# Kernel tuning notes

Measured on AMD Instinct MI355X. Metric: run time of the kernel, lower is better.

Reference implementation:

```python
import jax, jax.numpy as jnp
import numpy as np

B, S, D = 2, 4096, 1024
H, DK, DV = 4, 128, 256          # head_k_dim, head_v_dim
KD, VD = H * DK, H * DV          # key_dim=512, value_dim=1024
RANK = 16                        # gate_low_rank_dim
GLN = 16.0                       # gate_logit_normalizer
EPS = 1e-5
C = 64                           # chunk size
NC = S // C


def setup_inputs() -> dict:
    key = jax.random.key(0)
    ks = jax.random.split(key, 9)
    w = lambda k, shape: (jax.random.normal(k, shape, jnp.float32) * 0.02)
    return {
        "x": jax.random.normal(ks[0], (B, S, D), jnp.float32),
        "Wq": w(ks[1], (D, KD)),
        "Wk": w(ks[2], (D, KD)),
        "Wv": w(ks[3], (D, VD)),
        "Wgk1": w(ks[4], (D, RANK)),
        "Wgk2": w(ks[5], (RANK, KD)),
        "bgk": jnp.zeros((KD,), jnp.float32),
        "Wg": w(ks[6], (D, VD)),
        "Wo": w(ks[7], (VD, D)),
        "norm_w": jnp.ones((DV,), jnp.float32),
    }


def _gla_chunk(q, k, v, gk):
    """Chunkwise gated linear attention. q,k,gk: [B,S,H,DK]; v: [B,S,H,DV]."""
    qc = q.reshape(B, NC, C, H, DK)
    kc = k.reshape(B, NC, C, H, DK)
    vc = v.reshape(B, NC, C, H, DV)
    gc = gk.reshape(B, NC, C, H, DK)
    gcum = jnp.cumsum(gc, axis=2)                       # inclusive within-chunk cumsum (<= 0)
    g_last = gcum[:, :, -1]                             # [B,NC,H,DK]
    q_t = qc * jnp.exp(gcum)                            # q decayed forward
    k_inv = kc * jnp.exp(-gcum)                         # for intra-chunk scores
    k_dec = kc * jnp.exp(g_last[:, :, None] - gcum)     # for state update (bounded)
    # intra-chunk causal scores
    A = jnp.einsum('bnthk,bnshk->bnhts', q_t, k_inv)    # [B,NC,H,C,C]
    mask = jnp.tril(jnp.ones((C, C), bool))
    A = jnp.where(mask, A, 0.0)
    o_intra = jnp.einsum('bnhts,bnshv->bnthv', A, vc)   # [B,NC,C,H,DV]
    # per-chunk state contribution
    kv = jnp.einsum('bnthk,bnthv->bnhkv', k_dec, vc)    # [B,NC,H,DK,DV]

    def step(state, inp):
        q_tc, gl, kvc = inp                             # [B,C,H,DK], [B,H,DK], [B,H,DK,DV]
        o_inter = jnp.einsum('bthk,bhkv->bthv', q_tc, state)
        state = state * jnp.exp(gl)[..., None] + kvc
        return state, o_inter

    xs = (jnp.swapaxes(q_t, 0, 1), jnp.swapaxes(g_last, 0, 1), jnp.swapaxes(kv, 0, 1))
    init = jnp.zeros((B, H, DK, DV), q.dtype)
    _, o_inter = jax.lax.scan(step, init, xs)           # [NC,B,C,H,DV]
    o = o_intra + jnp.swapaxes(o_inter, 0, 1)
    return o.reshape(B, S, H, DV)


def reference(x, Wq, Wk, Wv, Wgk1, Wgk2, bgk, Wg, Wo, norm_w):
    scale = DK ** -0.5
    q = (x @ Wq).reshape(B, S, H, DK) * scale
    k = (x @ Wk).reshape(B, S, H, DK)
    v = (x @ Wv).reshape(B, S, H, DV)
    gk = (jax.nn.log_sigmoid((x @ Wgk1) @ Wgk2 + bgk) / GLN).reshape(B, S, H, DK)
    o = _gla_chunk(q, k, v, gk)                          # [B,S,H,DV]
    # fused RMSNorm + swish gate (per-head norm over DV)
    g = (x @ Wg).reshape(B, S, H, DV)
    o = o * jax.lax.rsqrt(jnp.mean(o * o, axis=-1, keepdims=True) + EPS) * norm_w
    o = o * (g * jax.nn.sigmoid(g))
    return o.reshape(B, S, VD) @ Wo
```

## Files before the change

kernel.cpp:

```cpp
#include <hip/hip_runtime.h>

typedef __bf16 bf16_t;
typedef __bf16 bf16x8 __attribute__((ext_vector_type(8)));
typedef float  f32x4  __attribute__((ext_vector_type(4)));

#define MFMA16(a,b,c) __builtin_amdgcn_mfma_f32_16x16x32_bf16((a),(b),(c),0,0,0)

#define SCALE_Q 0.08838834764831845f

#define GLOBAL_LOAD_LDS16(gptr, lptr)                                          \
  __builtin_amdgcn_global_load_lds(                                            \
      (const __attribute__((address_space(1))) void*)(gptr),                   \
      (__attribute__((address_space(3))) void*)(lptr), 16, 0, 0)

#define SBAR   __builtin_amdgcn_s_barrier()
#define SCHEDB __builtin_amdgcn_sched_barrier(0)

__global__ __launch_bounds__(256) void k_convert(const void* __restrict__ src,
                                                 const unsigned int* __restrict__ nwp,
                                                 bf16_t* __restrict__ dst, int n) {
  bool isf32 = (nwp[0] == 0x3F800000u);
  int g = blockIdx.x * 256 + threadIdx.x;
  int i = g * 8;
  if (i >= n) return;
  if (isf32) {
    const float4* s = (const float4*)src;
    float4 a = s[g * 2], b = s[g * 2 + 1];
    bf16x8 o;
    o[0] = (bf16_t)a.x; o[1] = (bf16_t)a.y; o[2] = (bf16_t)a.z; o[3] = (bf16_t)a.w;
    o[4] = (bf16_t)b.x; o[5] = (bf16_t)b.y; o[6] = (bf16_t)b.z; o[7] = (bf16_t)b.w;
    *(bf16x8*)(dst + i) = o;
  } else {
    *(bf16x8*)(dst + i) = ((const bf16x8*)src)[g];
  }
}

struct ConvSrcs {
  const void *wq, *wk, *wv, *wg, *wo, *gk1, *gk2, *bgk, *nw;
};
__device__ __forceinline__ void convT_tile(const void* src, bf16_t* dst,
                                           int Ccols, int bx, int by,
                                           bool isf32, bf16_t (*t)[33]) {
  int tx = threadIdx.x & 31, ty = threadIdx.x >> 5;
  int r0 = by * 32, c0 = bx * 32;
#pragma unroll
  for (int i = 0; i < 4; i++) {
    int r = r0 + ty + i * 8, cc = c0 + tx;
    float v = isf32 ? ((const float*)src)[(size_t)r * Ccols + cc]
                    : (float)((const bf16_t*)src)[(size_t)r * Ccols + cc];
    t[ty + i * 8][tx] = (bf16_t)v;
  }
  __syncthreads();
#pragma unroll
  for (int i = 0; i < 4; i++) {
    int cc = c0 + ty + i * 8;
    dst[(size_t)cc * 1024 + r0 + tx] = t[tx][ty + i * 8];
  }
}
__device__ __forceinline__ void conv_straight(const void* src, bf16_t* dst,
                                              int base_blk, int n, bool isf32) {
  int g = (blockIdx.x - base_blk) * 256 + threadIdx.x;
  int i = g * 8;
  if (i >= n) return;
  if (isf32) {
    const float4* s = (const float4*)src;
    float4 a = s[g * 2], b = s[g * 2 + 1];
    bf16x8 o;
    o[0] = (bf16_t)a.x; o[1] = (bf16_t)a.y; o[2] = (bf16_t)a.z; o[3] = (bf16_t)a.w;
    o[4] = (bf16_t)b.x; o[5] = (bf16_t)b.y; o[6] = (bf16_t)b.z; o[7] = (bf16_t)b.w;
    *(bf16x8*)(dst + i) = o;
  } else {
    *(bf16x8*)(dst + i) = ((const bf16x8*)src)[g];
  }
}
__global__ __launch_bounds__(256) void k_convW(ConvSrcs s,
                                               const unsigned int* __restrict__ nwp,
                                               bf16_t* __restrict__ tWcat,
                                               bf16_t* __restrict__ tWo,
                                               bf16_t* __restrict__ cWgk1,
                                               bf16_t* __restrict__ cWgk2,
                                               bf16_t* __restrict__ cbgk,
                                               bf16_t* __restrict__ cnw) {
  __shared__ bf16_t t[32][33];
  bool isf32 = (nwp[0] == 0x3F800000u);
  int blk = blockIdx.x;
  if (blk < 512) {
    convT_tile(s.wq, tWcat, 512, blk & 15, blk >> 4, isf32, t);
  } else if (blk < 1024) {
    int b2 = blk - 512;
    convT_tile(s.wk, tWcat + (size_t)512 * 1024, 512, b2 & 15, b2 >> 4, isf32, t);
  } else if (blk < 2048) {
    int b2 = blk - 1024;
    convT_tile(s.wv, tWcat + (size_t)1024 * 1024, 1024, b2 & 31, b2 >> 5, isf32, t);
  } else if (blk < 3072) {
    int b2 = blk - 2048;
    convT_tile(s.wg, tWcat + (size_t)2048 * 1024, 1024, b2 & 31, b2 >> 5, isf32, t);
  } else if (blk < 4096) {
    int b2 = blk - 3072;
    convT_tile(s.wo, tWo, 1024, b2 & 31, b2 >> 5, isf32, t);
  } else if (blk < 4104) {
    conv_straight(s.gk1, cWgk1, 4096, 16384, isf32);
  } else if (blk < 4108) {
    conv_straight(s.gk2, cWgk2, 4104, 8192, isf32);
  } else if (blk == 4108) {
    conv_straight(s.bgk, cbgk, 4108, 512, isf32);
  } else {
    conv_straight(s.nw, cnw, 4109, 256, isf32);
  }
}

__global__ __launch_bounds__(256) void k_gk1(const bf16_t* __restrict__ x,
                                             const bf16_t* __restrict__ W1,
                                             float* __restrict__ tmp) {
  int wave = threadIdx.x >> 6, lane = threadIdx.x & 63;
  int m = blockIdx.x * 4 + wave;
  const bf16_t* xr = x + (size_t)m * 1024;
  float p[16];
#pragma unroll
  for (int n = 0; n < 16; n++) p[n] = 0.f;
  for (int kk = 0; kk < 16; kk++) {
    int k = kk * 64 + lane;
    float xv = (float)xr[k];
    bf16x8 w0 = *(const bf16x8*)(W1 + k * 16);
    bf16x8 w1 = *(const bf16x8*)(W1 + k * 16 + 8);
#pragma unroll
    for (int j = 0; j < 8; j++) {
      p[j]     += xv * (float)w0[j];
      p[8 + j] += xv * (float)w1[j];
    }
  }
#pragma unroll
  for (int off = 1; off < 64; off <<= 1) {
#pragma unroll
    for (int n = 0; n < 16; n++) p[n] += __shfl_xor(p[n], off, 64);
  }
#pragma unroll
  for (int n = 0; n < 16; n++)
    if (lane == n) tmp[(size_t)m * 16 + n] = p[n];
}

__global__ __launch_bounds__(256) void k_gk2(const float* __restrict__ tmp,
                                             const bf16_t* __restrict__ W2,
                                             const bf16_t* __restrict__ bgk,
                                             float* __restrict__ gcum) {
  int g = blockIdx.x * 256 + threadIdx.x;
  int m = g >> 6;
  int n0 = (g & 63) * 8;
  float acc[8];
#pragma unroll
  for (int j = 0; j < 8; j++) acc[j] = 0.f;
  for (int k = 0; k < 16; k++) {
    float tv = tmp[(size_t)m * 16 + k];
    bf16x8 w = *(const bf16x8*)(W2 + k * 512 + n0);
#pragma unroll
    for (int j = 0; j < 8; j++) acc[j] += tv * (float)w[j];
  }
  int b = m >> 12, s = m & 4095;
  int h = n0 >> 7, dk0 = n0 & 127;
  float* dst = gcum + (((size_t)(b * 4 + h) * 4096 + s) * 128 + dk0);
#pragma unroll
  for (int j = 0; j < 8; j++) {
    float z = acc[j] + (float)bgk[n0 + j];
    float lg = -__logf(1.f + __expf(-z)) * (1.f / 16.f);
    dst[j] = fmaxf(lg, -4.0f);
  }
}

__global__ __launch_bounds__(128) void k_cumsum(float* __restrict__ gcum,
                                                float* __restrict__ glast) {
  int blk = blockIdx.x;
  int dk = threadIdx.x;
  float* base = gcum + (size_t)blk * 8192;
  float run = 0.f;
  for (int t = 0; t < 64; t++) {
    run += base[t * 128 + dk];
    base[t * 128 + dk] = run;
  }
  glast[(size_t)blk * 128 + dk] = run;
}

template <int BM, int BN, int NBN, int MODE>
__global__ __launch_bounds__(512, 2) void k_gemm2(
    const bf16_t* __restrict__ Ag, const bf16_t* __restrict__ Bt,
    const float* __restrict__ gcum, const float* __restrict__ glast,
    bf16_t* __restrict__ qt, bf16_t* __restrict__ kinv,
    bf16_t* __restrict__ kdec, bf16_t* __restrict__ vr,
    bf16_t* __restrict__ gmat, float* __restrict__ fout) {
  constexpr int MT = BM / 2 / 16;
  constexpr int ALDS = BM * 64;
  constexpr int BLDS = BN * 64;
  constexpr int NT = 16;
  extern __shared__ __attribute__((aligned(16))) bf16_t sm[];
  bf16_t* As = sm;
  bf16_t* Bs = sm + 2 * ALDS;

  int tid = threadIdx.x;
  int w = tid >> 6, lane = tid & 63;
  int WM = w >> 2, WN = w & 3;
  int quad = lane >> 4, c = lane & 15;

  int nblk = gridDim.x;
  int bid = blockIdx.x;
  int swz = (bid & 7) * (nblk >> 3) + (bid >> 3);
  int bm = swz / NBN, bn = swz % NBN;
  int m0 = bm * BM, n0 = bn * BN;

  int srow = w * 8 + (lane >> 3);
  int scol = ((lane & 7) ^ (lane >> 3)) * 8;
  const bf16_t* aBase = Ag + (size_t)(m0 + srow) * 1024 + scol;
  const bf16_t* bBase = Bt + (size_t)(n0 + srow) * 1024 + scol;

  auto stage = [&](int t, int buf) {
    int kof = t * 64;
#pragma unroll
    for (int j = 0; j < BM / 64; j++)
      GLOBAL_LOAD_LDS16(aBase + (size_t)j * 64 * 1024 + kof,
                        As + buf * ALDS + j * 4096 + w * 512);
#pragma unroll
    for (int j = 0; j < BN / 64; j++)
      GLOBAL_LOAD_LDS16(bBase + (size_t)j * 64 * 1024 + kof,
                        Bs + buf * BLDS + j * 4096 + w * 512);
  };

  int sx = c & 7;
  int aRowOff[MT], bRowOff[4];
#pragma unroll
  for (int mt = 0; mt < MT; mt++) aRowOff[mt] = (WM * (BM / 2) + mt * 16 + c) * 64;
#pragma unroll
  for (int nt = 0; nt < 4; nt++) bRowOff[nt] = (WN * 64 + nt * 16 + c) * 64;

  f32x4 acc[MT][4] = {};

  stage(0, 0);
  stage(1, 1);

  auto compute = [&](int buf) {
#pragma unroll
    for (int ks = 0; ks < 2; ks++) {
      int so = (((ks << 2) | quad) ^ sx) << 3;
      bf16x8 bfr[4];
#pragma unroll
      for (int nt = 0; nt < 4; nt++)
        bfr[nt] = *(const bf16x8*)(Bs + buf * BLDS + bRowOff[nt] + so);
#pragma unroll
      for (int mt = 0; mt < MT; mt++) {
        bf16x8 af = *(const bf16x8*)(As + buf * ALDS + aRowOff[mt] + so);
#pragma unroll
        for (int nt = 0; nt < 4; nt++)
          acc[mt][nt] = MFMA16(af, bfr[nt], acc[mt][nt]);
      }
    }
  };

#pragma unroll 2
  for (int t = 0; t < NT; t++) {
    if (t < NT - 1) {
      if constexpr (BM == 256)
        asm volatile("s_waitcnt vmcnt(8)" ::: "memory");
      else
        asm volatile("s_waitcnt vmcnt(6)" ::: "memory");
    } else {
      asm volatile("s_waitcnt vmcnt(0)" ::: "memory");
    }
    SCHEDB;
    SBAR;
    SCHEDB;
    __builtin_amdgcn_s_setprio(1);
    compute(t & 1);
    __builtin_amdgcn_s_setprio(0);
    SCHEDB;
    SBAR;
    SCHEDB;
    if (t + 2 < NT) stage(t + 2, t & 1);
  }

  int mwb = m0 + WM * (BM / 2);
  int nwb = n0 + WN * 64;
#pragma unroll
  for (int mt = 0; mt < MT; mt++)
#pragma unroll
    for (int nt = 0; nt < 4; nt++)
#pragma unroll
      for (int r = 0; r < 4; r++) {
        int m = mwb + mt * 16 + quad * 4 + r;
        int n = nwb + nt * 16 + c;
        float v = acc[mt][nt][r];
        if constexpr (MODE == 1) {
          fout[(size_t)m * 1024 + n] = v;
        } else {
          if (n0 < 512) {
            int b = m >> 12, ss = m & 4095, h = n >> 7, dk = n & 127;
            size_t idx = ((size_t)(b * 4 + h) * 4096 + ss) * 128 + dk;
            qt[idx] = (bf16_t)(v * SCALE_Q * __expf(gcum[idx]));
          } else if (n0 < 1024) {
            int nk = n - 512;
            int b = m >> 12, ss = m & 4095, h = nk >> 7, dk = nk & 127;
            size_t idx = ((size_t)(b * 4 + h) * 4096 + ss) * 128 + dk;
            float gc = gcum[idx];
            float gl = glast[((size_t)(b * 4 + h) * 64 + (ss >> 6)) * 128 + dk];
            kinv[idx] = (bf16_t)(v * __expf(fminf(-gc, 30.f)));
            kdec[idx] = (bf16_t)(v * __expf(gl - gc));
          } else if (n0 < 2048) {
            int nv = n - 1024;
            int b = m >> 12, ss = m & 4095, h = nv >> 8, dv = nv & 255;
            vr[((size_t)(b * 4 + h) * 4096 + ss) * 256 + dv] = (bf16_t)v;
          } else {
            gmat[(size_t)m * 1024 + (n - 2048)] = (bf16_t)v;
          }
        }
      }
}

__global__ __launch_bounds__(256) void k_attA(const bf16_t* __restrict__ qt,
                                              const bf16_t* __restrict__ kinv,
                                              bf16_t* __restrict__ Aout) {
  int blk = blockIdx.x;
  size_t cb = (size_t)blk * 8192;
  int tid = threadIdx.x, wave = tid >> 6, lane = tid & 63;
  int quad = lane >> 4, c = lane & 15;
  f32x4 acc[4] = {};
  for (int kk = 0; kk < 128; kk += 32) {
    bf16x8 a = *(const bf16x8*)(qt + cb + (size_t)(wave * 16 + c) * 128 + kk + quad * 8);
#pragma unroll
    for (int nt = 0; nt < 4; nt++) {
      bf16x8 bb = *(const bf16x8*)(kinv + cb + (size_t)(nt * 16 + c) * 128 + kk + quad * 8);
      acc[nt] = MFMA16(a, bb, acc[nt]);
    }
  }
#pragma unroll
  for (int nt = 0; nt < 4; nt++)
#pragma unroll
    for (int r = 0; r < 4; r++) {
      int row = wave * 16 + quad * 4 + r, col = nt * 16 + c;
      Aout[(size_t)blk * 4096 + row * 64 + col] =
          (bf16_t)(col <= row ? acc[nt][r] : 0.f);
    }
}

__global__ __launch_bounds__(256, 3) void k_kv(const bf16_t* __restrict__ kdec,
                                            const bf16_t* __restrict__ vr,
                                            bf16_t* __restrict__ kv) {
  int blk = blockIdx.x;
  __shared__ __attribute__((aligned(16))) bf16_t ls_kd[64 * 128];
  __shared__ __attribute__((aligned(16))) bf16_t ls_v[64 * 256];
  int tid = threadIdx.x, wave = tid >> 6, lane = tid & 63;
  int quad = lane >> 4, c = lane & 15;
  size_t cb = (size_t)blk * 8192;
  size_t cv = (size_t)blk * 16384;
  size_t sb = (size_t)blk * 32768;
#pragma unroll
  for (int j = 0; j < 4; j++) {
    int idx = tid + j * 256;
    int row = idx >> 4, col = (idx & 15) * 8;
    *(bf16x8*)&ls_kd[row * 128 + col] = *(const bf16x8*)(kdec + cb + (size_t)row * 128 + col);
  }
#pragma unroll
  for (int j = 0; j < 8; j++) {
    int idx = tid + j * 256;
    int row = idx >> 5, col = (idx & 31) * 8;
    *(bf16x8*)&ls_v[row * 256 + col] = *(const bf16x8*)(vr + cv + (size_t)row * 256 + col);
  }
  __syncthreads();
  int kbase = (wave >> 1) * 64;
  for (int pos = 0; pos < 2; pos++) {
    int dvbase = (wave & 1) * 64 + pos * 128;
    f32x4 acc[4][4] = {};
    for (int kk = 0; kk < 64; kk += 32) {
      bf16x8 a[4], bb[4];
#pragma unroll
      for (int mt = 0; mt < 4; mt++)
#pragma unroll
        for (int j = 0; j < 8; j++)
          a[mt][j] = ls_kd[(kk + quad * 8 + j) * 128 + kbase + mt * 16 + c];
#pragma unroll
      for (int nt = 0; nt < 4; nt++)
#pragma unroll
        for (int j = 0; j < 8; j++)
          bb[nt][j] = ls_v[(kk + quad * 8 + j) * 256 + dvbase + nt * 16 + c];
#pragma unroll
      for (int mt = 0; mt < 4; mt++)
#pragma unroll
        for (int nt = 0; nt < 4; nt++)
          acc[mt][nt] = MFMA16(a[mt], bb[nt], acc[mt][nt]);
    }
#pragma unroll
    for (int mt = 0; mt < 4; mt++)
#pragma unroll
      for (int nt = 0; nt < 4; nt++)
#pragma unroll
        for (int r = 0; r < 4; r++) {
          int kg = kbase + mt * 16 + quad * 4 + r;
          int dg = dvbase + nt * 16 + c;
          kv[sb + (size_t)kg * 256 + dg] = (bf16_t)acc[mt][nt][r];
        }
  }
}

__global__ __launch_bounds__(256) void k_scan2(bf16_t* __restrict__ states,
                                               const float* __restrict__ glast) {
  int g = blockIdx.x * 256 + threadIdx.x;
  int bh = g >> 15;
  int idx = g & 32767;
  int kg = idx >> 8;
  bf16_t* p = states + (size_t)bh * 64 * 32768 + idx;
  const float* gl = glast + (size_t)bh * 64 * 128 + kg;
  float carry = 0.f;
#pragma unroll 4
  for (int n = 0; n < 64; n++) {
    float kvv = (float)p[(size_t)n * 32768];
    float e = __expf(gl[n * 128]);
    p[(size_t)n * 32768] = (bf16_t)carry;
    carry = carry * e + kvv;
  }
}

__global__ __launch_bounds__(256, 4) void k_o(const bf16_t* __restrict__ qt,
                                           const bf16_t* __restrict__ Amat,
                                           const bf16_t* __restrict__ vr,
                                           const bf16_t* __restrict__ states,
                                           const bf16_t* __restrict__ gmat,
                                           const bf16_t* __restrict__ normw,
                                           bf16_t* __restrict__ ob) {
  int blk = blockIdx.x;
  int bh = blk >> 6, n = blk & 63, b = bh >> 2, h = bh & 3;
  __shared__ __attribute__((aligned(16))) bf16_t ls[64 * 256];
  __shared__ __attribute__((aligned(16))) float lred[64][4];
  int tid = threadIdx.x, wave = tid >> 6, lane = tid & 63;
  int quad = lane >> 4, c = lane & 15;
  size_t cb = (size_t)blk * 8192;
  size_t cv = (size_t)blk * 16384;
  size_t sb = (size_t)blk * 32768;
  f32x4 acc[4][4] = {};
  for (int half = 0; half < 2; half++) {
    __syncthreads();
#pragma unroll
    for (int i = 0; i < 8; i++) {
      int idx = tid + i * 256;
      int row = idx >> 5, col = (idx & 31) * 8;
      *(bf16x8*)&ls[row * 256 + col] =
          *(const bf16x8*)(states + sb + (size_t)(half * 64 + row) * 256 + col);
    }
    __syncthreads();
    for (int kk2 = 0; kk2 < 2; kk2++) {
      int kl = kk2 * 32, kg = half * 64 + kl;
      bf16x8 a[4], bb[4];
#pragma unroll
      for (int mt = 0; mt < 4; mt++)
        a[mt] = *(const bf16x8*)(qt + cb + (size_t)(mt * 16 + c) * 128 + kg + quad * 8);
#pragma unroll
      for (int nt = 0; nt < 4; nt++)
#pragma unroll
        for (int j = 0; j < 8; j++)
          bb[nt][j] = ls[(kl + quad * 8 + j) * 256 + wave * 64 + nt * 16 + c];
#pragma unroll
      for (int mt = 0; mt < 4; mt++)
#pragma unroll
        for (int nt = 0; nt < 4; nt++)
          acc[mt][nt] = MFMA16(a[mt], bb[nt], acc[mt][nt]);
    }
  }
  __syncthreads();
#pragma unroll
  for (int i = 0; i < 8; i++) {
    int idx = tid + i * 256;
    int row = idx >> 5, col = (idx & 31) * 8;
    *(bf16x8*)&ls[row * 256 + col] =
        *(const bf16x8*)(vr + cv + (size_t)row * 256 + col);
  }
  __syncthreads();
  for (int kk = 0; kk < 64; kk += 32) {
    bf16x8 a[4], bb[4];
#pragma unroll
    for (int mt = 0; mt < 4; mt++)
      a[mt] = *(const bf16x8*)(Amat + (size_t)blk * 4096 + (size_t)(mt * 16 + c) * 64 + kk + quad * 8);
#pragma unroll
    for (int nt = 0; nt < 4; nt++)
#pragma unroll
      for (int j = 0; j < 8; j++)
        bb[nt][j] = ls[(kk + quad * 8 + j) * 256 + wave * 64 + nt * 16 + c];
#pragma unroll
    for (int mt = 0; mt < 4; mt++)
#pragma unroll
      for (int nt = 0; nt < 4; nt++)
        acc[mt][nt] = MFMA16(a[mt], bb[nt], acc[mt][nt]);
  }
  float p[4][4];
#pragma unroll
  for (int mt = 0; mt < 4; mt++)
#pragma unroll
    for (int r = 0; r < 4; r++) {
      float s = 0.f;
#pragma unroll
      for (int nt = 0; nt < 4; nt++) s += acc[mt][nt][r] * acc[mt][nt][r];
      p[mt][r] = s;
    }
#pragma unroll
  for (int off = 1; off < 16; off <<= 1) {
#pragma unroll
    for (int mt = 0; mt < 4; mt++)
#pragma unroll
      for (int r = 0; r < 4; r++) p[mt][r] += __shfl_xor(p[mt][r], off, 64);
  }
  if (c == 0) {
#pragma unroll
    for (int mt = 0; mt < 4; mt++)
#pragma unroll
      for (int r = 0; r < 4; r++) lred[mt * 16 + quad * 4 + r][wave] = p[mt][r];
  }
  __syncthreads();
#pragma unroll
  for (int mt = 0; mt < 4; mt++)
#pragma unroll
    for (int r = 0; r < 4; r++) {
      int row = mt * 16 + quad * 4 + r;
      float tot = lred[row][0] + lred[row][1] + lred[row][2] + lred[row][3];
      float rs = rsqrtf(tot * (1.f / 256.f) + 1e-5f);
      int sg = n * 64 + row;
      size_t gb = ((size_t)(b * 4096 + sg)) * 1024 + h * 256;
#pragma unroll
      for (int nt = 0; nt < 4; nt++) {
        int dv = wave * 64 + nt * 16 + c;
        float ov = acc[mt][nt][r] * rs * (float)normw[dv];
        float gv = (float)gmat[gb + dv];
        ov *= gv / (1.f + __expf(-gv));
        ob[gb + dv] = (bf16_t)ov;
      }
    }
}

extern "C" void kernel_launch(void* const* d_in, const int* in_sizes, int n_in,
                              void* d_out, int out_size, void* d_ws, size_t ws_size,
                              hipStream_t stream) {
  (void)in_sizes; (void)n_in; (void)out_size; (void)ws_size;
  const unsigned int* nw_oracle = (const unsigned int*)d_in[9];

  static int attr_done = 0;
  if (!attr_done) {
    (void)hipFuncSetAttribute((const void*)&k_gemm2<256, 256, 12, 0>,
                              hipFuncAttributeMaxDynamicSharedMemorySize, 131072);
    (void)hipFuncSetAttribute((const void*)&k_gemm2<128, 256, 4, 1>,
                              hipFuncAttributeMaxDynamicSharedMemorySize, 98304);
    attr_done = 1;
  }

  char* ws = (char*)d_ws;
  size_t off = 0;
  auto alloc = [&](size_t bytes) -> void* {
    void* p = ws + off;
    off += (bytes + 255) & ~(size_t)255;
    return p;
  };
  bf16_t* states = (bf16_t*)alloc((size_t)512 * 32768 * 2);
  bf16_t* cx     = states;
  float*  glast  = (float*) alloc((size_t)8 * 64 * 128 * 4);
  float*  tmp    = (float*) alloc((size_t)8192 * 16 * 4);
  float*  gcum   = (float*) alloc((size_t)8 * 4096 * 128 * 4);
  bf16_t* ob     = (bf16_t*)gcum;
  bf16_t* qt     = (bf16_t*)alloc((size_t)8 * 4096 * 128 * 2);
  bf16_t* kinv   = (bf16_t*)alloc((size_t)8 * 4096 * 128 * 2);
  bf16_t* kdec   = (bf16_t*)alloc((size_t)8 * 4096 * 128 * 2);
  bf16_t* vr     = (bf16_t*)alloc((size_t)8 * 4096 * 256 * 2);
  bf16_t* gmat   = (bf16_t*)alloc((size_t)8192 * 1024 * 2);
  bf16_t* Amat   = (bf16_t*)alloc((size_t)512 * 4096 * 2);
  bf16_t* tWcat  = (bf16_t*)alloc((size_t)3072 * 1024 * 2);
  bf16_t* cWgk1  = (bf16_t*)alloc((size_t)1024 * 16 * 2);
  bf16_t* cWgk2  = (bf16_t*)alloc((size_t)16 * 512 * 2);
  bf16_t* cbgk   = (bf16_t*)alloc((size_t)512 * 2);
  bf16_t* tWo    = (bf16_t*)alloc((size_t)1024 * 1024 * 2);
  bf16_t* cnw    = (bf16_t*)alloc((size_t)256 * 2);

  k_convert<<<4096, 256, 0, stream>>>(d_in[0], nw_oracle, cx, 8192 * 1024);
  ConvSrcs cs{d_in[1], d_in[2], d_in[3], d_in[7], d_in[8],
              d_in[4], d_in[5], d_in[6], d_in[9]};
  k_convW<<<4110, 256, 0, stream>>>(cs, nw_oracle, tWcat, tWo,
                                    cWgk1, cWgk2, cbgk, cnw);

  k_gk1<<<2048, 256, 0, stream>>>(cx, cWgk1, tmp);
  k_gk2<<<2048, 256, 0, stream>>>(tmp, cWgk2, cbgk, gcum);
  k_cumsum<<<512, 128, 0, stream>>>(gcum, glast);
  k_gemm2<256, 256, 12, 0><<<384, 512, 131072, stream>>>(
      cx, tWcat, gcum, glast, qt, kinv, kdec, vr, gmat, nullptr);
  k_attA<<<512, 256, 0, stream>>>(qt, kinv, Amat);
  k_kv<<<512, 256, 0, stream>>>(kdec, vr, states);
  k_scan2<<<1024, 256, 0, stream>>>(states, glast);
  k_o<<<512, 256, 0, stream>>>(qt, Amat, vr, states, gmat, cnw, ob);
  k_gemm2<128, 256, 4, 1><<<256, 512, 98304, stream>>>(
      ob, tWo, nullptr, nullptr, nullptr, nullptr, nullptr, nullptr, nullptr,
      (float*)d_out);
}
```

Measured before the change: 349.3 us.

## Rewrite GEMM main loop with fine-grained interleaved load/MFMA phases and XCD-aware tile mapping

Replaces the two-stage stage/compute GEMM loop with a hand-scheduled loop. Each K-tile is split into four phases, and global-to-LDS loads for half-tiles are issued between MFMA bursts, with explicit vmcnt and lgkmcnt waits and barriers. Block-to-tile mapping is also changed so that blocks on the same XCD share A/B tiles for better L2 reuse. The goal is to hide memory latency behind compute in the projection and output GEMMs, at the cost of more barriers and complex waitcnt bookkeeping that could stall if it is miscounted.

```diff
diff --git a/kernel.cpp b/kernel.cpp
--- a/kernel.cpp
+++ b/kernel.cpp
@@ -15,6 +15,7 @@
 
 #define SBAR   __builtin_amdgcn_s_barrier()
 #define SCHEDB __builtin_amdgcn_sched_barrier(0)
+#define LGKM0  asm volatile("s_waitcnt lgkmcnt(0)" ::: "memory")
 
 __global__ __launch_bounds__(256) void k_convert(const void* __restrict__ src,
                                                  const unsigned int* __restrict__ nwp,
@@ -179,17 +180,19 @@
   glast[(size_t)blk * 128 + dk] = run;
 }
 
-template <int BM, int BN, int NBN, int MODE>
-__global__ __launch_bounds__(512, 2) void k_gemm2(
+template <int BM, int MODE>
+__global__ __launch_bounds__(512, 2) void k_gemm3(
     const bf16_t* __restrict__ Ag, const bf16_t* __restrict__ Bt,
     const float* __restrict__ gcum, const float* __restrict__ glast,
     bf16_t* __restrict__ qt, bf16_t* __restrict__ kinv,
     bf16_t* __restrict__ kdec, bf16_t* __restrict__ vr,
     bf16_t* __restrict__ gmat, float* __restrict__ fout) {
-  constexpr int MT = BM / 2 / 16;
+  constexpr int MT = BM / 32;
+  constexpr int HMT = MT / 2;
+  constexpr int LPW_A = BM / 128;
   constexpr int ALDS = BM * 64;
-  constexpr int BLDS = BN * 64;
-  constexpr int NT = 16;
+  constexpr int BLDS = 256 * 64;
+  constexpr int NI = 8;
   extern __shared__ __attribute__((aligned(16))) bf16_t sm[];
   bf16_t* As = sm;
   bf16_t* Bs = sm + 2 * ALDS;
@@ -199,80 +202,124 @@
   int WM = w >> 2, WN = w & 3;
   int quad = lane >> 4, c = lane & 15;
 
-  int nblk = gridDim.x;
   int bid = blockIdx.x;
-  int swz = (bid & 7) * (nblk >> 3) + (bid >> 3);
-  int bm = swz / NBN, bn = swz % NBN;
-  int m0 = bm * BM, n0 = bn * BN;
-
-  int srow = w * 8 + (lane >> 3);
-  int scol = ((lane & 7) ^ (lane >> 3)) * 8;
-  const bf16_t* aBase = Ag + (size_t)(m0 + srow) * 1024 + scol;
-  const bf16_t* bBase = Bt + (size_t)(n0 + srow) * 1024 + scol;
-
-  auto stage = [&](int t, int buf) {
-    int kof = t * 64;
-#pragma unroll
-    for (int j = 0; j < BM / 64; j++)
-      GLOBAL_LOAD_LDS16(aBase + (size_t)j * 64 * 1024 + kof,
-                        As + buf * ALDS + j * 4096 + w * 512);
-#pragma unroll
-    for (int j = 0; j < BN / 64; j++)
-      GLOBAL_LOAD_LDS16(bBase + (size_t)j * 64 * 1024 + kof,
-                        Bs + buf * BLDS + j * 4096 + w * 512);
-  };
-
-  int sx = c & 7;
-  int aRowOff[MT], bRowOff[4];
-#pragma unroll
-  for (int mt = 0; mt < MT; mt++) aRowOff[mt] = (WM * (BM / 2) + mt * 16 + c) * 64;
-#pragma unroll
-  for (int nt = 0; nt < 4; nt++) bRowOff[nt] = (WN * 64 + nt * 16 + c) * 64;
-
+  int xcd = bid & 7, bslot = bid >> 3;
+  int bm, bn;
+  if constexpr (MODE == 0) {
+    bm = (xcd >> 1) * 8 + (bslot & 7);
+    bn = (xcd & 1) * 6 + (bslot >> 3);
+  } else {
+    bm = xcd * 8 + (bslot & 7);
+    bn = bslot >> 3;
+  }
+  int m0 = bm * BM, n0 = bn * 256;
+
+  int srow = 8 * w + (lane >> 3);
+  int ssw = ((lane & 7) ^ ((lane >> 3) & 7)) * 8;
+  const bf16_t* aPp[2][2];
+  const bf16_t* bPp[2][2];
+#pragma unroll
+  for (int h = 0; h < 2; h++)
+#pragma unroll
+    for (int j = 0; j < 2; j++) {
+      aPp[h][j] = Ag + (size_t)(m0 + h * (BM / 2) + j * 64 + srow) * 1024 + ssw;
+      bPp[h][j] = Bt + (size_t)(n0 + h * 128 + j * 64 + srow) * 1024 + ssw;
+    }
+
+  int rowA[MT], rowB[4];
+#pragma unroll
+  for (int mtg = 0; mtg < MT; mtg++)
+    rowA[mtg] = (WM * (BM / 2) + mtg * 16 + c) * 64;
+#pragma unroll
+  for (int nt = 0; nt < 4; nt++) rowB[nt] = (WN * 64 + nt * 16 + c) * 64;
+  int so0 = (quad ^ (c & 7)) * 8;
+  int so1 = ((4 | quad) ^ (c & 7)) * 8;
+
+#define STA(H, KT, BUF)                                                        \
+  do {                                                                         \
+    GLOBAL_LOAD_LDS16(aPp[H][0] + (size_t)(KT) * 64,                           \
+                      As + (BUF) * ALDS + ((H) * (BM / 2) + 8 * w) * 64);      \
+    if constexpr (LPW_A == 2)                                                  \
+      GLOBAL_LOAD_LDS16(aPp[H][1] + (size_t)(KT) * 64,                         \
+                        As + (BUF) * ALDS + ((H) * (BM / 2) + 8 * w + 64) * 64); \
+  } while (0)
+#define STB(H, KT, BUF)                                                        \
+  do {                                                                         \
+    GLOBAL_LOAD_LDS16(bPp[H][0] + (size_t)(KT) * 64,                           \
+                      Bs + (BUF) * BLDS + ((H) * 128 + 8 * w) * 64);           \
+    GLOBAL_LOAD_LDS16(bPp[H][1] + (size_t)(KT) * 64,                           \
+                      Bs + (BUF) * BLDS + ((H) * 128 + 8 * w + 64) * 64);      \
+  } while (0)
+
+  bf16x8 af[HMT], bfr[4];
   f32x4 acc[MT][4] = {};
 
-  stage(0, 0);
-  stage(1, 1);
-
-  auto compute = [&](int buf) {
-#pragma unroll
-    for (int ks = 0; ks < 2; ks++) {
-      int so = (((ks << 2) | quad) ^ sx) << 3;
-      bf16x8 bfr[4];
-#pragma unroll
-      for (int nt = 0; nt < 4; nt++)
-        bfr[nt] = *(const bf16x8*)(Bs + buf * BLDS + bRowOff[nt] + so);
-#pragma unroll
-      for (int mt = 0; mt < MT; mt++) {
-        bf16x8 af = *(const bf16x8*)(As + buf * ALDS + aRowOff[mt] + so);
-#pragma unroll
-        for (int nt = 0; nt < 4; nt++)
-          acc[mt][nt] = MFMA16(af, bfr[nt], acc[mt][nt]);
-      }
-    }
-  };
-
-#pragma unroll 2
-  for (int t = 0; t < NT; t++) {
-    if (t < NT - 1) {
-      if constexpr (BM == 256)
-        asm volatile("s_waitcnt vmcnt(8)" ::: "memory");
-      else
-        asm volatile("s_waitcnt vmcnt(6)" ::: "memory");
-    } else {
-      asm volatile("s_waitcnt vmcnt(0)" ::: "memory");
-    }
-    SCHEDB;
-    SBAR;
-    SCHEDB;
-    __builtin_amdgcn_s_setprio(1);
-    compute(t & 1);
-    __builtin_amdgcn_s_setprio(0);
-    SCHEDB;
-    SBAR;
-    SCHEDB;
-    if (t + 2 < NT) stage(t + 2, t & 1);
-  }
+#define DSA(BUF, QA, SO)                                                       \
+  _Pragma("unroll") for (int mp = 0; mp < HMT; mp++)                           \
+      af[mp] = *(const bf16x8*)(As + (BUF) * ALDS + rowA[(QA) * HMT + mp] + (SO));
+#define DSB(BUF, SO)                                                           \
+  _Pragma("unroll") for (int nt = 0; nt < 4; nt++)                             \
+      bfr[nt] = *(const bf16x8*)(Bs + (BUF) * BLDS + rowB[nt] + (SO));
+#define MM(QA)                                                                 \
+  _Pragma("unroll") for (int mp = 0; mp < HMT; mp++)                           \
+  _Pragma("unroll") for (int nt = 0; nt < 4; nt++)                             \
+      acc[(QA) * HMT + mp][nt] =                                               \
+          MFMA16(af[mp], bfr[nt], acc[(QA) * HMT + mp][nt]);
+#define PH_MID                                                                 \
+  SCHEDB; SBAR; LGKM0; SCHEDB; __builtin_amdgcn_s_setprio(1)
+#define PH_END                                                                 \
+  __builtin_amdgcn_s_setprio(0); SCHEDB; SBAR; SCHEDB
+
+  STA(0, 0, 0); STA(1, 0, 0); STB(0, 0, 0); STB(1, 0, 0);
+  STB(0, 1, 1);
+  asm volatile("s_waitcnt vmcnt(2)" ::: "memory");
+  SCHEDB; SBAR; SCHEDB;
+
+#pragma unroll 1
+  for (int i = 0; i < NI; i++) {
+    int kt = 2 * i;
+    bool nl = (i < NI - 1);
+    DSA(0, 0, so0); DSB(0, so0);
+    STA(0, kt + 1, 1);
+    PH_MID; MM(0); PH_END;
+    DSA(0, 1, so0);
+    STA(1, kt + 1, 1);
+    PH_MID; MM(1); PH_END;
+    DSA(0, 0, so1); DSB(0, so1);
+    STB(1, kt + 1, 1);
+    PH_MID; MM(0); PH_END;
+    DSA(0, 1, so1);
+    if (nl) STB(0, kt + 2, 0);
+    PH_MID; MM(1);
+    __builtin_amdgcn_s_setprio(0); SCHEDB;
+    if (i == NI - 1) { asm volatile("s_waitcnt vmcnt(0)" ::: "memory"); }
+    else             { asm volatile("s_waitcnt vmcnt(2)" ::: "memory"); }
+    SCHEDB; SBAR; SCHEDB;
+    DSA(1, 0, so0); DSB(1, so0);
+    if (nl) STA(0, kt + 2, 0);
+    PH_MID; MM(0); PH_END;
+    DSA(1, 1, so0);
+    if (nl) STA(1, kt + 2, 0);
+    PH_MID; MM(1); PH_END;
+    DSA(1, 0, so1); DSB(1, so1);
+    if (nl) STB(1, kt + 2, 0);
+    PH_MID; MM(0); PH_END;
+    DSA(1, 1, so1);
+    if (nl) STB(0, kt + 3, 1);
+    PH_MID; MM(1);
+    __builtin_amdgcn_s_setprio(0); SCHEDB;
+    if (nl) {
+      asm volatile("s_waitcnt vmcnt(2)" ::: "memory");
+      SCHEDB; SBAR; SCHEDB;
+    }
+  }
+#undef STA
+#undef STB
+#undef DSA
+#undef DSB
+#undef MM
+#undef PH_MID
+#undef PH_END
 
   int mwb = m0 + WM * (BM / 2);
   int nwb = n0 + WN * 64;
@@ -536,9 +583,9 @@
 
   static int attr_done = 0;
   if (!attr_done) {
-    (void)hipFuncSetAttribute((const void*)&k_gemm2<256, 256, 12, 0>,
+    (void)hipFuncSetAttribute((const void*)&k_gemm3<256, 0>,
                               hipFuncAttributeMaxDynamicSharedMemorySize, 131072);
-    (void)hipFuncSetAttribute((const void*)&k_gemm2<128, 256, 4, 1>,
+    (void)hipFuncSetAttribute((const void*)&k_gemm3<128, 1>,
                               hipFuncAttributeMaxDynamicSharedMemorySize, 98304);
     attr_done = 1;
   }
@@ -578,13 +625,13 @@
   k_gk1<<<2048, 256, 0, stream>>>(cx, cWgk1, tmp);
   k_gk2<<<2048, 256, 0, stream>>>(tmp, cWgk2, cbgk, gcum);
   k_cumsum<<<512, 128, 0, stream>>>(gcum, glast);
-  k_gemm2<256, 256, 12, 0><<<384, 512, 131072, stream>>>(
+  k_gemm3<256, 0><<<384, 512, 131072, stream>>>(
       cx, tWcat, gcum, glast, qt, kinv, kdec, vr, gmat, nullptr);
   k_attA<<<512, 256, 0, stream>>>(qt, kinv, Amat);
   k_kv<<<512, 256, 0, stream>>>(kdec, vr, states);
   k_scan2<<<1024, 256, 0, stream>>>(states, glast);
   k_o<<<512, 256, 0, stream>>>(qt, Amat, vr, states, gmat, cnw, ob);
-  k_gemm2<128, 256, 4, 1><<<256, 512, 98304, stream>>>(
+  k_gemm3<128, 1><<<256, 512, 98304, stream>>>(
       ob, tWo, nullptr, nullptr, nullptr, nullptr, nullptr, nullptr, nullptr,
       (float*)d_out);
 }
```

Measured after the change: 375.3 us. 7.5% more time.
